# Optimization experiments

Measured on AMD Instinct MI355X. Metric: run time of the kernel, lower is better.

Reference implementation:

```python
import jax, jax.numpy as jnp
import numpy as np

D_MODEL, D_STATE, D_INNER, DT_RANK, D_CONV, K = 768, 16, 1536, 48, 3, 2
B_SZ, L_SEQ = 2, 2048

def setup_inputs() -> dict:
    key = jax.random.key(0)
    ks = jax.random.split(key, 10)
    s = lambda k, shp, sc=0.02: jax.random.normal(k, shp, dtype=jnp.float32) * sc
    return {
        "x": jax.random.normal(ks[0], (B_SZ, L_SEQ, D_MODEL), dtype=jnp.float32),
        "in_proj_w": s(ks[1], (2 * D_INNER, D_MODEL)),
        "conv_w": s(ks[2], (D_INNER, 1, D_CONV), 0.3),
        "conv_b": s(ks[3], (D_INNER,), 0.1),
        "x_proj_w": s(ks[4], (K, DT_RANK + 2 * D_STATE, D_INNER)),
        "dt_proj_w": s(ks[5], (K, D_INNER, DT_RANK), 0.1),
        "dt_proj_b": s(ks[6], (K, D_INNER), 0.1),
        "A_logs": s(ks[7], (K * D_INNER, D_STATE), 0.5),
        "Ds": jnp.ones((K * D_INNER,), dtype=jnp.float32),
        "out_proj_w": s(ks[8], (D_MODEL, D_INNER)),
    }

def _selective_scan(u, delta, A, Bp, Cp, Dk):
    # u, delta: [B, L, D]; A: [D, N]; Bp, Cp: [B, L, N]; Dk: [D]
    def step(h, inp):
        d_t, u_t, b_t, c_t = inp  # [B,D], [B,D], [B,N], [B,N]
        dA = jnp.exp(d_t[..., None] * A)  # [B,D,N]
        h = h * dA + (d_t * u_t)[..., None] * b_t[:, None, :]
        y_t = jnp.einsum('bdn,bn->bd', h, c_t)
        return h, y_t
    h0 = jnp.zeros((u.shape[0], u.shape[2], A.shape[1]), dtype=u.dtype)
    xs = (jnp.swapaxes(delta, 0, 1), jnp.swapaxes(u, 0, 1),
          jnp.swapaxes(Bp, 0, 1), jnp.swapaxes(Cp, 0, 1))
    _, ys = jax.lax.scan(step, h0, xs)  # ys: [L, B, D]
    return jnp.swapaxes(ys, 0, 1) + u * Dk  # [B, L, D]

def _direction(u_k, xw_k, dtw_k, dtb_k, Alog_k, D_k):
    x_dbl = jnp.einsum('bld,rd->blr', u_k, xw_k)
    dt_in, Bp, Cp = jnp.split(x_dbl, [DT_RANK, DT_RANK + D_STATE], axis=-1)
    delta = jax.nn.softplus(jnp.einsum('blr,dr->bld', dt_in, dtw_k) + dtb_k)
    A = -jnp.exp(Alog_k)
    return _selective_scan(u_k, delta, A, Bp, Cp, D_k)

def reference(x, in_proj_w, conv_w, conv_b, x_proj_w, dt_proj_w, dt_proj_b, A_logs, Ds, out_proj_w):
    xz = x @ in_proj_w.T                       # [B, L, 2*Din]
    x_conv, z = jnp.split(xz, 2, axis=-1)
    xc = jnp.swapaxes(x_conv, 1, 2)            # [B, Din, L]
    pad = (D_CONV - 1) // 2
    xc = jax.lax.conv_general_dilated(
        xc, conv_w, window_strides=(1,), padding=[(pad, pad)],
        feature_group_count=D_INNER, dimension_numbers=('NCH', 'OIH', 'NCH'))
    xc = xc + conv_b[None, :, None]
    u = jnp.swapaxes(jax.nn.silu(xc), 1, 2)    # [B, L, Din]

    u_dirs = jnp.stack([u, jnp.flip(u, axis=1)])          # [K, B, L, Din]
    A_logs_k = A_logs.reshape(K, D_INNER, D_STATE)
    Ds_k = Ds.reshape(K, D_INNER)
    y_dirs = jax.vmap(_direction)(u_dirs, x_proj_w, dt_proj_w, dt_proj_b, A_logs_k, Ds_k)
    y_scanned = y_dirs[0] + jnp.flip(y_dirs[1], axis=1)
    y_gated = y_scanned * z
    return y_gated @ out_proj_w.T
```

## Files before the change

kernel.cpp:

```cpp
#include <hip/hip_runtime.h>
#include <math.h>

#define D_MODEL 768
#define D_STATE 16
#define D_INNER 1536
#define DT_RANK 48
#define B_SZ    2
#define L_SEQ   2048
#define CH      64
#define NCH     (L_SEQ / CH)
#define NDG     24
#define MTOT    (B_SZ * L_SEQ)
#define LOG2E   1.4426950408889634f
#define LN2     0.6931471805599453f

typedef __bf16 bf16x8 __attribute__((ext_vector_type(8)));
typedef float f32x4 __attribute__((ext_vector_type(4)));
typedef ushort ushort8_t __attribute__((ext_vector_type(8)));

__device__ __forceinline__ float ex2(float x) {
  return __builtin_amdgcn_exp2f(x);
}

__device__ __forceinline__ ushort f2bf(float f) {
  unsigned int u = __float_as_uint(f);
  unsigned int r = (u + 0x7fff + ((u >> 16) & 1)) >> 16;
  return (ushort)r;
}
__device__ __forceinline__ float bf2f(ushort u) {
  return __uint_as_float(((unsigned int)u) << 16);
}

__device__ __forceinline__ void gload_lds16(const ushort* g, ushort* l) {
  __builtin_amdgcn_global_load_lds(
      (__attribute__((address_space(1))) void*)(void*)(g),
      (__attribute__((address_space(3))) void*)(void*)(l), 16, 0, 0);
}

__device__ __forceinline__ float softplus_fast(float x) {
  return (x > 20.f) ? x : LN2 * __log2f(1.f + ex2(x * LOG2E));
}

template <int BM, int BN, int ACT, int OBF, int DTOUT>
__device__ __forceinline__ void gemm_body(
    const ushort* __restrict__ A, int lda, const ushort* __restrict__ B,
    int ldb, const float* __restrict__ bias, void* __restrict__ Cp, int ldc,
    int Nreal, int K, int bxi, int byi, ushort* __restrict__ dtin) {
  __shared__ ushort As[2][BM][32];
  __shared__ ushort Bs[2][BN][32];
  constexpr int WM = BM / 2, WN = BN / 2;
  constexpr int FM = WM / 16, FN = WN / 16;
  const int tid = threadIdx.x;
  const int lane = tid & 63;
  const int w = tid >> 6;
  const int wr = w >> 1, wc = w & 1;
  const int bm = byi * BM, bn = bxi * BN;
  const int lrow = lane >> 2;
  const int lchunk = lane & 3;
  const int fr = lane & 15;
  const int k8 = (lane >> 4) * 8;

  f32x4 acc[FM][FN] = {};

  auto stage = [&](int buf, int k0) {
#pragma unroll
    for (int g = 0; g < BM / 64; ++g) {
      const int rb = w * (BM / 4) + g * 16;
      gload_lds16(A + (size_t)(bm + rb + lrow) * lda + k0 + lchunk * 8,
                  &As[buf][rb][0]);
    }
#pragma unroll
    for (int g = 0; g < BN / 64; ++g) {
      const int rb = w * (BN / 4) + g * 16;
      gload_lds16(B + (size_t)(bn + rb + lrow) * ldb + k0 + lchunk * 8,
                  &Bs[buf][rb][0]);
    }
  };

  stage(0, 0);
  __syncthreads();
  int cur = 0;
  for (int k0 = 0; k0 < K; k0 += 32) {
    if (k0 + 32 < K) stage(cur ^ 1, k0 + 32);
    bf16x8 af[FM], bfr[FN];
#pragma unroll
    for (int m = 0; m < FM; ++m)
      af[m] =
          *reinterpret_cast<const bf16x8*>(&As[cur][wr * WM + m * 16 + fr][k8]);
#pragma unroll
    for (int n = 0; n < FN; ++n)
      bfr[n] =
          *reinterpret_cast<const bf16x8*>(&Bs[cur][wc * WN + n * 16 + fr][k8]);
#pragma unroll
    for (int m = 0; m < FM; ++m)
#pragma unroll
      for (int n = 0; n < FN; ++n)
        acc[m][n] = __builtin_amdgcn_mfma_f32_16x16x32_bf16(af[m], bfr[n],
                                                            acc[m][n], 0, 0, 0);
    __syncthreads();
    cur ^= 1;
  }

  const int row4 = (lane >> 4) * 4;
#pragma unroll
  for (int m = 0; m < FM; ++m) {
#pragma unroll
    for (int n = 0; n < FN; ++n) {
      const int gn = bn + wc * WN + n * 16 + fr;
      const int gm0 = bm + wr * WM + m * 16 + row4;
#pragma unroll
      for (int j = 0; j < 4; ++j) {
        const float v = acc[m][n][j];
        const int gm = gm0 + j;
        if (DTOUT) {
          if (gn < 64)
            dtin[(size_t)gm * 64 + gn] = (gn < 48) ? f2bf(v) : (ushort)0;
          else if (gn >= 80 && gn < 144)
            dtin[(size_t)MTOT * 64 + (size_t)gm * 64 + (gn - 80)] =
                (gn < 128) ? f2bf(v) : (ushort)0;
        }
        if (gn < Nreal) {
          float vv = v + (bias ? bias[gn] : 0.f);
          if (ACT == 1) vv = softplus_fast(vv);
          if (OBF)
            ((ushort*)Cp)[(size_t)gm * ldc + gn] = f2bf(vv);
          else
            ((float*)Cp)[(size_t)gm * ldc + gn] = vv;
        }
      }
    }
  }
}

template <int BM, int BN, int ACT, int OBF, int DTOUT>
__global__ __launch_bounds__(256) void gemm_k(
    const ushort* __restrict__ A, int lda, const ushort* __restrict__ B,
    int ldb, const float* __restrict__ bias, void* __restrict__ Cp, int ldc,
    int Nreal, int K, ushort* __restrict__ dtin) {
  gemm_body<BM, BN, ACT, OBF, DTOUT>(A, lda, B, ldb, bias, Cp, ldc, Nreal, K,
                                     blockIdx.x, blockIdx.y, dtin);
}

__global__ __launch_bounds__(256) void gemm_dt_k(
    const ushort* __restrict__ dtin, const ushort* __restrict__ w_dt,
    const float* __restrict__ dtb, ushort* __restrict__ delta) {
  const int k = blockIdx.z;
  gemm_body<64, 128, 1, 1, 0>(
      dtin + (size_t)k * MTOT * 64, 64, w_dt + (size_t)k * D_INNER * 64, 64,
      dtb + k * D_INNER, delta + (size_t)k * MTOT * D_INNER, D_INNER, D_INNER,
      64, blockIdx.x, blockIdx.y, nullptr);
}

__global__ __launch_bounds__(256) void cvt_all_kernel(
    const float* __restrict__ x, const float* __restrict__ w_in,
    const float* __restrict__ w_out, const float* __restrict__ w_xp,
    const float* __restrict__ w_dt, ushort* __restrict__ x_bf,
    ushort* __restrict__ w_in_bf, ushort* __restrict__ w_out_bf,
    ushort* __restrict__ w_xp_bf, ushort* __restrict__ w_dt_bf) {
  const long N0 = 3145728, N1 = 2359296, N2 = 1179648, N3 = 393216, N4 = 196608;
  long i = ((long)blockIdx.x * 256 + threadIdx.x) * 4;
  if (i < N0) {
    const float4 v = *(const float4*)(x + i);
    ushort4 o = {f2bf(v.x), f2bf(v.y), f2bf(v.z), f2bf(v.w)};
    *(ushort4*)(x_bf + i) = o;
    return;
  }
  i -= N0;
  if (i < N1) {
    const float4 v = *(const float4*)(w_in + i);
    ushort4 o = {f2bf(v.x), f2bf(v.y), f2bf(v.z), f2bf(v.w)};
    *(ushort4*)(w_in_bf + i) = o;
    return;
  }
  i -= N1;
  if (i < N2) {
    const float4 v = *(const float4*)(w_out + i);
    ushort4 o = {f2bf(v.x), f2bf(v.y), f2bf(v.z), f2bf(v.w)};
    *(ushort4*)(w_out_bf + i) = o;
    return;
  }
  i -= N2;
  if (i < N3) {
    const long row = i / 1536;
    ushort4 o = {0, 0, 0, 0};
    if (row < 160) {
      const float4 v = *(const float4*)(w_xp + i);
      o.x = f2bf(v.x); o.y = f2bf(v.y); o.z = f2bf(v.z); o.w = f2bf(v.w);
    }
    *(ushort4*)(w_xp_bf + i) = o;
    return;
  }
  i -= N3;
  if (i < N4) {
    const int col = (int)(i & 63);
    const long row = i >> 6;
    ushort4 o = {0, 0, 0, 0};
    if (col < 48) {
      const float4 v = *(const float4*)(w_dt + row * 48 + col);
      o.x = f2bf(v.x); o.y = f2bf(v.y); o.z = f2bf(v.z); o.w = f2bf(v.w);
    }
    *(ushort4*)(w_dt_bf + i) = o;
  }
}

__global__ __launch_bounds__(256) void conv_silu_kernel(
    const ushort* __restrict__ xz, const float* __restrict__ cw,
    const float* __restrict__ cb, ushort* __restrict__ u_bf) {
  const int nd8 = D_INNER / 8;
  const int idx = blockIdx.x * 256 + threadIdx.x;
  const int d8 = idx % nd8;
  const int lg = (idx / nd8) % (L_SEQ / 8);
  const int b = idx / (nd8 * (L_SEQ / 8));
  const int d = d8 * 8;
  const int l0 = lg * 8;

  float w0[8], w1[8], w2[8], bs[8];
#pragma unroll
  for (int j = 0; j < 8; ++j) {
    w0[j] = cw[(d + j) * 3 + 0];
    w1[j] = cw[(d + j) * 3 + 1];
    w2[j] = cw[(d + j) * 3 + 2];
    bs[j] = cb[d + j];
  }
  const ushort* base = xz + ((size_t)b * L_SEQ) * 3072 + d;
  const ushort8_t zv = {0, 0, 0, 0, 0, 0, 0, 0};
  ushort8_t prev = (l0 > 0) ? *(const ushort8_t*)(base + (size_t)(l0 - 1) * 3072) : zv;
  ushort8_t curv = *(const ushort8_t*)(base + (size_t)l0 * 3072);
#pragma unroll
  for (int i = 0; i < 8; ++i) {
    const int l = l0 + i;
    const ushort8_t nxt =
        (l + 1 < L_SEQ) ? *(const ushort8_t*)(base + (size_t)(l + 1) * 3072) : zv;
    ushort8_t o;
#pragma unroll
    for (int j = 0; j < 8; ++j) {
      const float a = bs[j] + bf2f(prev[j]) * w0[j] + bf2f(curv[j]) * w1[j] +
                      bf2f(nxt[j]) * w2[j];
      o[j] = f2bf(a / (1.f + __expf(-a)));
    }
    *(ushort8_t*)(u_bf + ((size_t)b * L_SEQ + l) * D_INNER + d) = o;
    prev = curv;
    curv = nxt;
  }
}

__global__ __launch_bounds__(256) void scan_local_kernel(
    const ushort* __restrict__ u_bf, const float* __restrict__ xdbl,
    const ushort* __restrict__ delta_bf, const float* __restrict__ A_logs,
    const float* __restrict__ Ds, ushort* __restrict__ y,
    float* __restrict__ hfin, float* __restrict__ Tsum) {
  __shared__ float sd[32][64], su[32][64], sB[32][16], sC[32][16];
  const int tid = threadIdx.x;
  const int lane = tid & 63;
  const int w = tid >> 6;
  const int c = lane & 15;
  const int nq = lane >> 4;
  const int bid = blockIdx.x;
  const int ch = bid & (NCH - 1);
  const int rest = bid >> 5;
  const int dgB = rest % NDG;
  const int kb = rest / NDG;
  const int b = kb & 1;
  const int k = kb >> 1;
  const int d0 = dgB * 64;
  const int dl = w * 16 + c;
  const int d = d0 + dl;
  const int row = k * D_INNER + d;

  const float4 alv = *(const float4*)(A_logs + (size_t)row * D_STATE + nq * 4);
  const float An0 = -__expf(alv.x) * LOG2E, An1 = -__expf(alv.y) * LOG2E;
  const float An2 = -__expf(alv.z) * LOG2E, An3 = -__expf(alv.w) * LOG2E;
  const float Dk = Ds[row];

  const ushort* uptr = u_bf + ((size_t)b * L_SEQ) * D_INNER;
  const ushort* dptr = delta_bf + ((size_t)(k * B_SZ + b) * L_SEQ) * D_INNER;
  const float* xptr = xdbl + ((size_t)b * L_SEQ) * 160 + k * 80;
  ushort* yptr = y + ((size_t)(k * B_SZ + b) * L_SEQ) * D_INNER;

  const int r_st = tid >> 3, seg = tid & 7;
  const int ridx_st = k ? (31 - r_st) : r_st;
  const int t2 = tid & 127;
  const int rBC = t2 >> 2;
  const int ridx_bc = k ? (31 - rBC) : rBC;
  const int c4 = (t2 & 3) * 4;
  const bool isB = tid < 128;

  ushort8_t dv, uv;
  float4 bc;
  auto gload = [&](int sub) {
    const int t0 = ch * CH + sub * 32;
    const int lbase = k ? (L_SEQ - 32 - t0) : t0;
    const size_t off = (size_t)(lbase + r_st) * D_INNER + d0 + seg * 8;
    dv = *(const ushort8_t*)(dptr + off);
    uv = *(const ushort8_t*)(uptr + off);
    const size_t rowL = (size_t)(lbase + rBC);
    bc = isB ? *(const float4*)(xptr + rowL * 160 + DT_RANK + c4)
             : *(const float4*)(xptr + rowL * 160 + DT_RANK + D_STATE + c4);
  };

  gload(0);

  float h0 = 0.f, h1 = 0.f, h2 = 0.f, h3 = 0.f, S = 0.f;

  for (int sub = 0; sub < CH / 32; ++sub) {
    *(float4*)&sd[ridx_st][seg * 8] =
        make_float4(bf2f(dv[0]), bf2f(dv[1]), bf2f(dv[2]), bf2f(dv[3]));
    *(float4*)&sd[ridx_st][seg * 8 + 4] =
        make_float4(bf2f(dv[4]), bf2f(dv[5]), bf2f(dv[6]), bf2f(dv[7]));
    *(float4*)&su[ridx_st][seg * 8] =
        make_float4(bf2f(uv[0]), bf2f(uv[1]), bf2f(uv[2]), bf2f(uv[3]));
    *(float4*)&su[ridx_st][seg * 8 + 4] =
        make_float4(bf2f(uv[4]), bf2f(uv[5]), bf2f(uv[6]), bf2f(uv[7]));
    if (isB)
      *(float4*)&sB[ridx_bc][c4] = bc;
    else
      *(float4*)&sC[ridx_bc][c4] = bc;
    __syncthreads();
    if (sub + 1 < CH / 32) gload(sub + 1);
    const int t0 = ch * CH + sub * 32;
    for (int s = 0; s < 32; ++s) {
      const float dlt = sd[s][dl];
      const float uu = su[s][dl];
      S += dlt;
      const float4 Bv = *(const float4*)&sB[s][nq * 4];
      const float4 Cv = *(const float4*)&sC[s][nq * 4];
      const float du = dlt * uu;
      h0 = h0 * ex2(dlt * An0) + du * Bv.x;
      h1 = h1 * ex2(dlt * An1) + du * Bv.y;
      h2 = h2 * ex2(dlt * An2) + du * Bv.z;
      h3 = h3 * ex2(dlt * An3) + du * Bv.w;
      float yt = h0 * Cv.x + h1 * Cv.y + h2 * Cv.z + h3 * Cv.w;
      yt += __shfl_xor(yt, 16);
      yt += __shfl_xor(yt, 32);
      if (nq == 0) {
        const int t = t0 + s;
        const int l = k ? (L_SEQ - 1 - t) : t;
        yptr[(size_t)l * D_INNER + d] = f2bf(yt + uu * Dk);
      }
    }
    __syncthreads();
  }

  const size_t cidxB = ((size_t)(k * B_SZ + b) * NCH + ch) * NDG + dgB;
  *(float4*)(hfin + cidxB * 1024 + dl * 16 + nq * 4) =
      make_float4(h0, h1, h2, h3);
  if (nq == 0) Tsum[cidxB * 64 + dl] = S;
}

__global__ __launch_bounds__(256) void scan_stitch_kernel(
    const float* __restrict__ hfin, const float* __restrict__ Tsum,
    const float* __restrict__ A_logs, float* __restrict__ hin) {
  const int tid = threadIdx.x;
  const int dl = tid >> 2;
  const int nq = tid & 3;
  const int bid = blockIdx.x;
  const int dgB = bid % NDG;
  const int b = (bid / NDG) & 1;
  const int k = bid / (NDG * 2);
  const int row = k * D_INNER + dgB * 64 + dl;
  const float4 alv = *(const float4*)(A_logs + (size_t)row * D_STATE + nq * 4);
  const float An0 = -__expf(alv.x) * LOG2E, An1 = -__expf(alv.y) * LOG2E;
  const float An2 = -__expf(alv.z) * LOG2E, An3 = -__expf(alv.w) * LOG2E;
  float c0 = 0.f, c1 = 0.f, c2 = 0.f, c3 = 0.f;
  for (int ch = 0; ch < NCH; ++ch) {
    const size_t cidxB = ((size_t)(k * B_SZ + b) * NCH + ch) * NDG + dgB;
    const size_t off = cidxB * 1024 + dl * 16 + nq * 4;
    *(float4*)(hin + off) = make_float4(c0, c1, c2, c3);
    const float T = Tsum[cidxB * 64 + dl];
    const float4 hf = *(const float4*)(hfin + off);
    c0 = c0 * ex2(An0 * T) + hf.x;
    c1 = c1 * ex2(An1 * T) + hf.y;
    c2 = c2 * ex2(An2 * T) + hf.z;
    c3 = c3 * ex2(An3 * T) + hf.w;
  }
}

__global__ __launch_bounds__(256) void fixup_gate_kernel(
    const float* __restrict__ xdbl, const ushort* __restrict__ delta_bf,
    const float* __restrict__ A_logs, const float* __restrict__ hin,
    const ushort* __restrict__ y, const ushort* __restrict__ xz_bf,
    ushort* __restrict__ yg) {
  __shared__ float sd0[64][64], sd1[64][64];
  __shared__ float sC0[64][16], sC1[64][16];
  __shared__ float sQF[64][4], sQB[64][4];
  const int tid = threadIdx.x;
  const int tq = tid >> 6;
  const int dl = tid & 63;
  const int bid = blockIdx.x;
  const int ch = bid & (NCH - 1);
  const int rest = bid >> 5;
  const int dgB = rest % NDG;
  const int b = rest / NDG;
  const int d0 = dgB * 64;
  const int d = d0 + dl;
  const int lbase = ch * CH;
  const int chb = NCH - 1 - ch;

  float AnF[16], AnB[16], hF[16], hB[16];
#pragma unroll
  for (int q = 0; q < 4; ++q) {
    const float4 af = *(const float4*)(A_logs + (size_t)d * D_STATE + q * 4);
    AnF[q * 4 + 0] = -__expf(af.x) * LOG2E;
    AnF[q * 4 + 1] = -__expf(af.y) * LOG2E;
    AnF[q * 4 + 2] = -__expf(af.z) * LOG2E;
    AnF[q * 4 + 3] = -__expf(af.w) * LOG2E;
    const float4 ab =
        *(const float4*)(A_logs + (size_t)(D_INNER + d) * D_STATE + q * 4);
    AnB[q * 4 + 0] = -__expf(ab.x) * LOG2E;
    AnB[q * 4 + 1] = -__expf(ab.y) * LOG2E;
    AnB[q * 4 + 2] = -__expf(ab.z) * LOG2E;
    AnB[q * 4 + 3] = -__expf(ab.w) * LOG2E;
  }
  const size_t cF = ((size_t)(0 * B_SZ + b) * NCH + ch) * NDG + dgB;
  const size_t cB = ((size_t)(1 * B_SZ + b) * NCH + chb) * NDG + dgB;
#pragma unroll
  for (int q = 0; q < 4; ++q) {
    const float4 hv = *(const float4*)(hin + cF * 1024 + dl * 16 + q * 4);
    hF[q * 4 + 0] = hv.x; hF[q * 4 + 1] = hv.y;
    hF[q * 4 + 2] = hv.z; hF[q * 4 + 3] = hv.w;
    const float4 hw = *(const float4*)(hin + cB * 1024 + dl * 16 + q * 4);
    hB[q * 4 + 0] = hw.x; hB[q * 4 + 1] = hw.y;
    hB[q * 4 + 2] = hw.z; hB[q * 4 + 3] = hw.w;
  }

  const ushort* d0p =
      delta_bf + ((size_t)(0 * B_SZ + b) * L_SEQ + lbase) * D_INNER + d0;
  const ushort* d1p =
      delta_bf + ((size_t)(1 * B_SZ + b) * L_SEQ + lbase) * D_INNER + d0;
#pragma unroll
  for (int i = 0; i < 2; ++i) {
    const int unit = tid + i * 256;
    const int r = unit >> 3, seg = unit & 7;
    const ushort8_t v0 =
        *(const ushort8_t*)(d0p + (size_t)r * D_INNER + seg * 8);
    const ushort8_t v1 =
        *(const ushort8_t*)(d1p + (size_t)r * D_INNER + seg * 8);
    *(float4*)&sd0[r][seg * 8] =
        make_float4(bf2f(v0[0]), bf2f(v0[1]), bf2f(v0[2]), bf2f(v0[3]));
    *(float4*)&sd0[r][seg * 8 + 4] =
        make_float4(bf2f(v0[4]), bf2f(v0[5]), bf2f(v0[6]), bf2f(v0[7]));
    *(float4*)&sd1[r][seg * 8] =
        make_float4(bf2f(v1[0]), bf2f(v1[1]), bf2f(v1[2]), bf2f(v1[3]));
    *(float4*)&sd1[r][seg * 8 + 4] =
        make_float4(bf2f(v1[4]), bf2f(v1[5]), bf2f(v1[6]), bf2f(v1[7]));
  }
  {
    const int r = tid >> 2;
    const int c4 = (tid & 3) * 4;
    const float* xrow = xdbl + ((size_t)b * L_SEQ + lbase + r) * 160;
    *(float4*)&sC0[r][c4] = *(const float4*)(xrow + DT_RANK + D_STATE + c4);
    *(float4*)&sC1[r][c4] =
        *(const float4*)(xrow + 80 + DT_RANK + D_STATE + c4);
  }
  __syncthreads();
  float qf = 0.f, qb = 0.f;
#pragma unroll
  for (int i = 0; i < 16; ++i) {
    qf += sd0[tq * 16 + i][dl];
    qb += sd1[tq * 16 + i][dl];
  }
  sQF[dl][tq] = qf;
  sQB[dl][tq] = qb;
  __syncthreads();
  float SF = 0.f, SB = 0.f;
#pragma unroll
  for (int j = 0; j < 4; ++j) {
    if (j < tq) SF += sQF[dl][j];
    if (j > tq) SB += sQB[dl][j];
  }

  const ushort* y0p = y + ((size_t)(0 * B_SZ + b) * L_SEQ) * D_INNER;
  const ushort* y1p = y + ((size_t)(1 * B_SZ + b) * L_SEQ) * D_INNER;
  float yacc[16];
#pragma unroll
  for (int i = 0; i < 16; ++i) {
    const int t = tq * 16 + i;
    SF += sd0[t][dl];
    float wf = 0.f;
#pragma unroll
    for (int n = 0; n < 16; ++n)
      wf += sC0[t][n] * (ex2(AnF[n] * SF) * hF[n]);
    yacc[i] = bf2f(y0p[(size_t)(lbase + t) * D_INNER + d]) + wf;
  }
#pragma unroll
  for (int i = 15; i >= 0; --i) {
    const int t = tq * 16 + i;
    SB += sd1[t][dl];
    float wb = 0.f;
#pragma unroll
    for (int n = 0; n < 16; ++n)
      wb += sC1[t][n] * (ex2(AnB[n] * SB) * hB[n]);
    yacc[i] += bf2f(y1p[(size_t)(lbase + t) * D_INNER + d]) + wb;
  }
#pragma unroll
  for (int i = 0; i < 16; ++i) {
    const int l = lbase + tq * 16 + i;
    const float z = bf2f(xz_bf[((size_t)b * L_SEQ + l) * 3072 + 1536 + d]);
    yg[((size_t)b * L_SEQ + l) * D_INNER + d] = f2bf(yacc[i] * z);
  }
}

extern "C" void kernel_launch(void* const* d_in, const int* in_sizes, int n_in,
                              void* d_out, int out_size, void* d_ws,
                              size_t ws_size, hipStream_t stream) {
  const float* x          = (const float*)d_in[0];
  const float* in_proj_w  = (const float*)d_in[1];
  const float* conv_w     = (const float*)d_in[2];
  const float* conv_b     = (const float*)d_in[3];
  const float* x_proj_w   = (const float*)d_in[4];
  const float* dt_proj_w  = (const float*)d_in[5];
  const float* dt_proj_b  = (const float*)d_in[6];
  const float* A_logs     = (const float*)d_in[7];
  const float* Ds         = (const float*)d_in[8];
  const float* out_proj_w = (const float*)d_in[9];
  float* out = (float*)d_out;

  const int M = MTOT;
  const size_t NST = (size_t)2 * B_SZ * NCH * NDG;

  float* ws    = (float*)d_ws;
  float* xdbl  = ws;
  float* hfin  = xdbl + (size_t)M * 160;
  float* hin   = hfin + NST * 1024;
  float* Tsum  = hin + NST * 1024;
  ushort* x_bf     = (ushort*)(Tsum + NST * 64);
  ushort* w_in_bf  = x_bf + (size_t)M * 768;
  ushort* w_out_bf = w_in_bf + (size_t)3072 * 768;
  ushort* w_xp_bf  = w_out_bf + (size_t)768 * 1536;
  ushort* w_dt_bf  = w_xp_bf + (size_t)256 * 1536;
  ushort* xz_bf    = w_dt_bf + (size_t)2 * 1536 * 64;
  ushort* u_bf     = xz_bf + (size_t)M * 3072;
  ushort* delta_bf = u_bf + (size_t)M * 1536;
  ushort* dtin     = delta_bf + (size_t)2 * M * 1536;
  ushort* y_bf     = dtin + (size_t)2 * M * 64;
  ushort* yg_bf    = y_bf + (size_t)2 * M * 1536;

  dim3 blk(256);

  {
    const long TOT = 3145728L + 2359296 + 1179648 + 393216 + 196608;
    cvt_all_kernel<<<dim3((TOT / 4 + 255) / 256), blk, 0, stream>>>(
        x, in_proj_w, out_proj_w, x_proj_w, dt_proj_w, x_bf, w_in_bf, w_out_bf,
        w_xp_bf, w_dt_bf);
  }

  gemm_k<128, 128, 0, 1, 0><<<dim3(3072 / 128, M / 128), blk, 0, stream>>>(
      x_bf, 768, w_in_bf, 768, nullptr, xz_bf, 3072, 3072, 768, nullptr);

  conv_silu_kernel<<<dim3(B_SZ * (L_SEQ / 8) * (D_INNER / 8) / 256), blk, 0,
                     stream>>>(xz_bf, conv_w, conv_b, u_bf);

  gemm_k<64, 64, 0, 0, 1><<<dim3(3, M / 64), blk, 0, stream>>>(
      u_bf, 1536, w_xp_bf, 1536, nullptr, xdbl, 160, 160, 1536, dtin);

  gemm_dt_k<<<dim3(1536 / 128, M / 64, 2), blk, 0, stream>>>(
      dtin, w_dt_bf, dt_proj_b, delta_bf);

  scan_local_kernel<<<dim3(2 * B_SZ * NDG * NCH), blk, 0, stream>>>(
      u_bf, xdbl, delta_bf, A_logs, Ds, y_bf, hfin, Tsum);
  scan_stitch_kernel<<<dim3(2 * B_SZ * NDG), blk, 0, stream>>>(hfin, Tsum,
                                                               A_logs, hin);
  fixup_gate_kernel<<<dim3(B_SZ * NDG * NCH), blk, 0, stream>>>(
      xdbl, delta_bf, A_logs, hin, y_bf, xz_bf, yg_bf);

  gemm_k<128, 128, 0, 0, 0><<<dim3(768 / 128, M / 128), blk, 0, stream>>>(
      yg_bf, 1536, w_out_bf, 1536, nullptr, out, 768, 768, 1536, nullptr);
}
```

Measured before the change: 228.7 us.

## Restructure local scan to 8 states per thread with async bf16 LDS staging

New measurement: 223.2 us. -2.4%, faster.

```diff
diff --git a/kernel.cpp b/kernel.cpp
--- a/kernel.cpp
+++ b/kernel.cpp
@@ -63,11 +63,17 @@
   f32x4 acc[FM][FN] = {};
 
   auto stage = [&](int buf, int k0) {
-#pragma unroll
-    for (int g = 0; g < BM / 64; ++g) {
-      const int rb = w * (BM / 4) + g * 16;
-      gload_lds16(A + (size_t)(bm + rb + lrow) * lda + k0 + lchunk * 8,
-                  &As[buf][rb][0]);
+    if constexpr (BM >= 64) {
+#pragma unroll
+      for (int g = 0; g < BM / 64; ++g) {
+        const int rb = w * (BM / 4) + g * 16;
+        gload_lds16(A + (size_t)(bm + rb + lrow) * lda + k0 + lchunk * 8,
+                    &As[buf][rb][0]);
+      }
+    } else {
+      if (w < 2)
+        gload_lds16(A + (size_t)(bm + w * 16 + lrow) * lda + k0 + lchunk * 8,
+                    &As[buf][w * 16][0]);
     }
 #pragma unroll
     for (int g = 0; g < BN / 64; ++g) {
@@ -244,17 +250,19 @@
   }
 }
 
-__global__ __launch_bounds__(256) void scan_local_kernel(
+__global__ __launch_bounds__(128) void scan_local_kernel(
     const ushort* __restrict__ u_bf, const float* __restrict__ xdbl,
     const ushort* __restrict__ delta_bf, const float* __restrict__ A_logs,
     const float* __restrict__ Ds, ushort* __restrict__ y,
     float* __restrict__ hfin, float* __restrict__ Tsum) {
-  __shared__ float sd[32][64], su[32][64], sB[32][16], sC[32][16];
+  __shared__ ushort sdu[32][64];
+  __shared__ ushort suu[32][64];
+  __shared__ float sB[32][16], sC[32][16];
   const int tid = threadIdx.x;
   const int lane = tid & 63;
   const int w = tid >> 6;
-  const int c = lane & 15;
-  const int nq = lane >> 4;
+  const int chW = lane >> 1;
+  const int half = lane & 1;
   const int bid = blockIdx.x;
   const int ch = bid & (NCH - 1);
   const int rest = bid >> 5;
@@ -263,13 +271,21 @@
   const int b = kb & 1;
   const int k = kb >> 1;
   const int d0 = dgB * 64;
-  const int dl = w * 16 + c;
+  const int dl = w * 32 + chW;
   const int d = d0 + dl;
   const int row = k * D_INNER + d;
 
-  const float4 alv = *(const float4*)(A_logs + (size_t)row * D_STATE + nq * 4);
-  const float An0 = -__expf(alv.x) * LOG2E, An1 = -__expf(alv.y) * LOG2E;
-  const float An2 = -__expf(alv.z) * LOG2E, An3 = -__expf(alv.w) * LOG2E;
+  float An[8];
+  {
+    const float4 a0 =
+        *(const float4*)(A_logs + (size_t)row * D_STATE + half * 8);
+    const float4 a1 =
+        *(const float4*)(A_logs + (size_t)row * D_STATE + half * 8 + 4);
+    An[0] = -__expf(a0.x) * LOG2E; An[1] = -__expf(a0.y) * LOG2E;
+    An[2] = -__expf(a0.z) * LOG2E; An[3] = -__expf(a0.w) * LOG2E;
+    An[4] = -__expf(a1.x) * LOG2E; An[5] = -__expf(a1.y) * LOG2E;
+    An[6] = -__expf(a1.z) * LOG2E; An[7] = -__expf(a1.w) * LOG2E;
+  }
   const float Dk = Ds[row];
 
   const ushort* uptr = u_bf + ((size_t)b * L_SEQ) * D_INNER;
@@ -277,62 +293,56 @@
   const float* xptr = xdbl + ((size_t)b * L_SEQ) * 160 + k * 80;
   ushort* yptr = y + ((size_t)(k * B_SZ + b) * L_SEQ) * D_INNER;
 
-  const int r_st = tid >> 3, seg = tid & 7;
-  const int ridx_st = k ? (31 - r_st) : r_st;
-  const int t2 = tid & 127;
-  const int rBC = t2 >> 2;
-  const int ridx_bc = k ? (31 - rBC) : rBC;
-  const int c4 = (t2 & 3) * 4;
-  const bool isB = tid < 128;
-
-  ushort8_t dv, uv;
-  float4 bc;
-  auto gload = [&](int sub) {
+  float h[8] = {};
+  float S = 0.f;
+
+  for (int sub = 0; sub < CH / 32; ++sub) {
     const int t0 = ch * CH + sub * 32;
     const int lbase = k ? (L_SEQ - 32 - t0) : t0;
-    const size_t off = (size_t)(lbase + r_st) * D_INNER + d0 + seg * 8;
-    dv = *(const ushort8_t*)(dptr + off);
-    uv = *(const ushort8_t*)(uptr + off);
-    const size_t rowL = (size_t)(lbase + rBC);
-    bc = isB ? *(const float4*)(xptr + rowL * 160 + DT_RANK + c4)
-             : *(const float4*)(xptr + rowL * 160 + DT_RANK + D_STATE + c4);
-  };
-
-  gload(0);
-
-  float h0 = 0.f, h1 = 0.f, h2 = 0.f, h3 = 0.f, S = 0.f;
-
-  for (int sub = 0; sub < CH / 32; ++sub) {
-    *(float4*)&sd[ridx_st][seg * 8] =
-        make_float4(bf2f(dv[0]), bf2f(dv[1]), bf2f(dv[2]), bf2f(dv[3]));
-    *(float4*)&sd[ridx_st][seg * 8 + 4] =
-        make_float4(bf2f(dv[4]), bf2f(dv[5]), bf2f(dv[6]), bf2f(dv[7]));
-    *(float4*)&su[ridx_st][seg * 8] =
-        make_float4(bf2f(uv[0]), bf2f(uv[1]), bf2f(uv[2]), bf2f(uv[3]));
-    *(float4*)&su[ridx_st][seg * 8 + 4] =
-        make_float4(bf2f(uv[4]), bf2f(uv[5]), bf2f(uv[6]), bf2f(uv[7]));
-    if (isB)
-      *(float4*)&sB[ridx_bc][c4] = bc;
-    else
-      *(float4*)&sC[ridx_bc][c4] = bc;
+    {
+      const ushort* src = (w == 0) ? dptr : uptr;
+      ushort* dst = (w == 0) ? &sdu[0][0] : &suu[0][0];
+#pragma unroll
+      for (int i = 0; i < 4; ++i) {
+        const int rd = i * 8 + (lane >> 3);
+        const int gr = k ? (31 - rd) : rd;
+        const int seg = lane & 7;
+        gload_lds16(src + (size_t)(lbase + gr) * D_INNER + d0 + seg * 8,
+                    dst + i * 512);
+      }
+    }
+    {
+      const int r = lane >> 1;
+      const int ridx = k ? (31 - r) : r;
+      const int c8 = (lane & 1) * 8;
+      const float* srcx =
+          xptr + (size_t)(lbase + r) * 160 + DT_RANK + (w ? D_STATE : 0) + c8;
+      float* dstx = (w == 0) ? &sB[ridx][c8] : &sC[ridx][c8];
+      *(float4*)dstx = *(const float4*)srcx;
+      *(float4*)(dstx + 4) = *(const float4*)(srcx + 4);
+    }
     __syncthreads();
-    if (sub + 1 < CH / 32) gload(sub + 1);
-    const int t0 = ch * CH + sub * 32;
     for (int s = 0; s < 32; ++s) {
-      const float dlt = sd[s][dl];
-      const float uu = su[s][dl];
+      const float dlt = bf2f(sdu[s][dl]);
+      const float uu = bf2f(suu[s][dl]);
       S += dlt;
-      const float4 Bv = *(const float4*)&sB[s][nq * 4];
-      const float4 Cv = *(const float4*)&sC[s][nq * 4];
       const float du = dlt * uu;
-      h0 = h0 * ex2(dlt * An0) + du * Bv.x;
-      h1 = h1 * ex2(dlt * An1) + du * Bv.y;
-      h2 = h2 * ex2(dlt * An2) + du * Bv.z;
-      h3 = h3 * ex2(dlt * An3) + du * Bv.w;
-      float yt = h0 * Cv.x + h1 * Cv.y + h2 * Cv.z + h3 * Cv.w;
-      yt += __shfl_xor(yt, 16);
-      yt += __shfl_xor(yt, 32);
-      if (nq == 0) {
+      const float4 Bv0 = *(const float4*)&sB[s][half * 8];
+      const float4 Bv1 = *(const float4*)&sB[s][half * 8 + 4];
+      const float4 Cv0 = *(const float4*)&sC[s][half * 8];
+      const float4 Cv1 = *(const float4*)&sC[s][half * 8 + 4];
+      h[0] = h[0] * ex2(dlt * An[0]) + du * Bv0.x;
+      h[1] = h[1] * ex2(dlt * An[1]) + du * Bv0.y;
+      h[2] = h[2] * ex2(dlt * An[2]) + du * Bv0.z;
+      h[3] = h[3] * ex2(dlt * An[3]) + du * Bv0.w;
+      h[4] = h[4] * ex2(dlt * An[4]) + du * Bv1.x;
+      h[5] = h[5] * ex2(dlt * An[5]) + du * Bv1.y;
+      h[6] = h[6] * ex2(dlt * An[6]) + du * Bv1.z;
+      h[7] = h[7] * ex2(dlt * An[7]) + du * Bv1.w;
+      float yt = h[0] * Cv0.x + h[1] * Cv0.y + h[2] * Cv0.z + h[3] * Cv0.w +
+                 h[4] * Cv1.x + h[5] * Cv1.y + h[6] * Cv1.z + h[7] * Cv1.w;
+      yt += __shfl_xor(yt, 1);
+      if (half == 0) {
         const int t = t0 + s;
         const int l = k ? (L_SEQ - 1 - t) : t;
         yptr[(size_t)l * D_INNER + d] = f2bf(yt + uu * Dk);
@@ -342,9 +352,11 @@
   }
 
   const size_t cidxB = ((size_t)(k * B_SZ + b) * NCH + ch) * NDG + dgB;
-  *(float4*)(hfin + cidxB * 1024 + dl * 16 + nq * 4) =
-      make_float4(h0, h1, h2, h3);
-  if (nq == 0) Tsum[cidxB * 64 + dl] = S;
+  *(float4*)(hfin + cidxB * 1024 + dl * 16 + half * 8) =
+      make_float4(h[0], h[1], h[2], h[3]);
+  *(float4*)(hfin + cidxB * 1024 + dl * 16 + half * 8 + 4) =
+      make_float4(h[4], h[5], h[6], h[7]);
+  if (half == 0) Tsum[cidxB * 64 + dl] = S;
 }
 
 __global__ __launch_bounds__(256) void scan_stitch_kernel(
@@ -536,6 +548,7 @@
   ushort* yg_bf    = y_bf + (size_t)2 * M * 1536;
 
   dim3 blk(256);
+  dim3 blk128(128);
 
   {
     const long TOT = 3145728L + 2359296 + 1179648 + 393216 + 196608;
@@ -550,13 +563,13 @@
   conv_silu_kernel<<<dim3(B_SZ * (L_SEQ / 8) * (D_INNER / 8) / 256), blk, 0,
                      stream>>>(xz_bf, conv_w, conv_b, u_bf);
 
-  gemm_k<64, 64, 0, 0, 1><<<dim3(3, M / 64), blk, 0, stream>>>(
+  gemm_k<32, 64, 0, 0, 1><<<dim3(3, M / 32), blk, 0, stream>>>(
       u_bf, 1536, w_xp_bf, 1536, nullptr, xdbl, 160, 160, 1536, dtin);
 
   gemm_dt_k<<<dim3(1536 / 128, M / 64, 2), blk, 0, stream>>>(
       dtin, w_dt_bf, dt_proj_b, delta_bf);
 
-  scan_local_kernel<<<dim3(2 * B_SZ * NDG * NCH), blk, 0, stream>>>(
+  scan_local_kernel<<<dim3(2 * B_SZ * NDG * NCH), blk128, 0, stream>>>(
       u_bf, xdbl, delta_bf, A_logs, Ds, y_bf, hfin, Tsum);
   scan_stitch_kernel<<<dim3(2 * B_SZ * NDG), blk, 0, stream>>>(hfin, Tsum,
                                                                A_logs, hin);
```
